# Optimization experiments

Measured on AMD Instinct MI355X. Metric: run time of the kernel, lower is better.

## Reference

```python
import jax, jax.numpy as jnp
import numpy as np

B, S, C, H, W = 8, 32, 3, 256, 256


def setup_inputs() -> dict:
    key = jax.random.key(0)
    k1, k2 = jax.random.split(key)
    return {
        "input": jax.random.normal(k1, (B, S, C, H, W), dtype=jnp.float32),
        "target": jax.random.normal(k2, (B, C, H, W), dtype=jnp.float32),
    }


def _l2norm(x, axis):
    # F.normalize: x / max(||x||_2, eps)
    return x / jnp.maximum(jnp.linalg.norm(x, axis=axis, keepdims=True), 1e-12)


def _forward(input, target):
    b, s, c, h, w = input.shape
    # target: [B,C,H,W] -> permute(0,1,3,2) -> [B,C,W,H] -> flatten(1,2) -> [B, C*W, H]
    target_f = _l2norm(jnp.transpose(target, (0, 1, 3, 2)).reshape(b, c * w, h), axis=1)
    # input: [B,S,C,H,W] -> permute(0,1,2,4,3) -> [B,S,C,W,H] -> flatten(2,3) -> [B,S,C*W,H]
    input_f = _l2norm(jnp.transpose(input, (0, 1, 2, 4, 3)).reshape(b, s, c * w, h), axis=2)

    def corr_one(xf, wf):
        # xf: [S, C*W, H] as conv batch, wf: [C*W, H] as single-output-channel kernel
        y = jax.lax.conv_general_dilated(
            xf, wf[None], window_strides=(1,), padding=[(h - 1, h - 1)],
            dimension_numbers=("NCH", "OIH", "NCH"))
        return y[:, 0, :h]  # first H shift positions (overlap sizes 1..H)

    corr = jax.vmap(corr_one)(input_f, target_f)  # [B, S, H]
    corr = corr / jnp.arange(1, h + 1, dtype=input.dtype)  # mean over overlap size

    overlap = jnp.argmax(corr, axis=-1)            # [B, S] best overlap per sample
    shift = (h - 1) - overlap                      # rows to shift up by

    # out[b,s,:,r,:] = input[b,s,:,r+shift,:] for r < overlap, else 0
    h_idx = jnp.arange(h)[None, None, :] + shift[:, :, None]  # [B, S, H]
    valid = h_idx < h
    idx = jnp.clip(h_idx, 0, h - 1)[:, :, None, :, None]      # [B,S,1,H,1]
    gathered = jnp.take_along_axis(input, idx, axis=3)
    return jnp.where(valid[:, :, None, :, None], gathered, jnp.zeros((), input.dtype))


def reference(input, target):
    return _forward(input, target)
```

## Files before the change

### kernel.cpp

```cpp
#include <hip/hip_runtime.h>

#define B_ 8
#define S_ 32
#define C_ 3
#define H_ 256
#define W_ 256
#define HW_ (H_*W_)
#define CHW_ (C_*H_*W_)
#define NT_ 24
#define TILE_ELEMS 8192

typedef __attribute__((ext_vector_type(8))) short bf16x8;
typedef __attribute__((ext_vector_type(4))) float f32x4;
typedef unsigned int u32;
typedef u32 __attribute__((address_space(3)))* lds_u32p;
typedef const u32 __attribute__((address_space(1)))* glb_u32p;

__device__ __forceinline__ void split2(float x, float y, unsigned &hp, unsigned &lp) {
  unsigned ux = __float_as_uint(x), uy = __float_as_uint(y);
  unsigned hx = ux & 0xFFFF0000u, hy = uy & 0xFFFF0000u;
  float lx = x - __uint_as_float(hx);
  float ly = y - __uint_as_float(hy);
  hp = (ux >> 16) | hy;
  lp = (__float_as_uint(lx) >> 16) | (__float_as_uint(ly) & 0xFFFF0000u);
}

__device__ __forceinline__ void gl2lds16(const ushort* g, ushort* l) {
  __builtin_amdgcn_global_load_lds((glb_u32p)g, (lds_u32p)l, 16, 0, 0);
}

__global__ void ct_ntg(const float* __restrict__ target, float* __restrict__ rntg) {
  int r = (int)((blockIdx.x * (size_t)blockDim.x + threadIdx.x) >> 6);
  int lane = threadIdx.x & 63;
  const float* base = target + (size_t)(r >> 8) * CHW_ + (size_t)(r & 255) * W_;
  float ss = 0.f;
#pragma unroll
  for (int c = 0; c < C_; ++c)
#pragma unroll
    for (int tt = 0; tt < W_/64; ++tt) {
      float v = base[c*HW_ + tt*64 + lane];
      ss = fmaf(v, v, ss);
    }
#pragma unroll
  for (int off = 32; off; off >>= 1) ss += __shfl_xor(ss, off);
  if (lane == 0) rntg[r] = 1.0f / fmaxf(sqrtf(ss), 1e-12f);
}

__global__ void ct_bsplit(const float* __restrict__ target,
                          ushort* __restrict__ BhG, ushort* __restrict__ BlG) {
  int bx = blockIdx.x;
  int b  = bx / 24, kt = bx % 24;
  int c  = kt >> 3, w0 = (kt & 7) * 32;
  int t  = threadIdx.x;
  int trow = t >> 3, tw = t & 7;
  const float* base = target + (size_t)(b*C_ + c) * HW_ + w0 + tw*4;
  ushort* oh = BhG + (size_t)bx * TILE_ELEMS;
  ushort* ol = BlG + (size_t)bx * TILE_ELEMS;
#pragma unroll
  for (int i = 0; i < 8; ++i) {
    int row = trow + 32*i;
    float4 v = *(const float4*)(base + (size_t)row * W_);
    unsigned h0, l0, h1, l1;
    split2(v.x, v.y, h0, l0); split2(v.z, v.w, h1, l1);
    int idx = (row>>4)*512 + (tw>>1)*128 + (row&15)*8 + (tw&1)*4;
    *(uint2*)&oh[idx] = make_uint2(h0, h1);
    *(uint2*)&ol[idx] = make_uint2(l0, l1);
  }
}

__global__ __launch_bounds__(512)
void ct_corr_mfma(const float* __restrict__ input,
                  const ushort* __restrict__ BhG, const ushort* __restrict__ BlG,
                  const float* __restrict__ rntg_g,
                  int* __restrict__ shift_out) {
  __shared__ ushort AhL[2][TILE_ELEMS], AlL[2][TILE_ELEMS];
  __shared__ ushort BhL[2][TILE_ELEMS], BlL[2][TILE_ELEMS];
  __shared__ float ninSq[256], rnin[256], rntg_s[256], corrS[256];
  __shared__ unsigned long long wkey[4];

  const int bs = blockIdx.x;
  const int bG = bs >> 5;
  const int t  = threadIdx.x;
  const int lane = t & 63;
  const int wid  = t >> 6;
  const int wm   = wid >> 2;
  const int wn   = wid & 3;

  const float* Abase = input + (size_t)bs * CHW_;

  if (t < 256) { ninSq[t] = 0.f; corrS[t] = 0.f; rntg_s[t] = rntg_g[bG*256 + t]; }

  f32x4 acc[8][4];
#pragma unroll
  for (int m = 0; m < 8; ++m)
#pragma unroll
    for (int n = 0; n < 4; ++n) acc[m][n] = (f32x4){0.f, 0.f, 0.f, 0.f};

  float4 paE[4], paO[4];
  float ssA[4] = {0.f, 0.f, 0.f, 0.f};

#define ISSUE_A(KT, PA) {                                                     \
    const float* Ab = Abase + (size_t)((KT) >> 3) * HW_ + ((KT) & 7) * 32;    \
    _Pragma("unroll")                                                         \
    for (int p = 0; p < 4; ++p) {                                             \
      int f = p*512 + t;                                                      \
      int row = (f >> 7) * 16 + ((f >> 1) & 15);                              \
      int kk  = ((f >> 5) & 3) * 8 + (f & 1) * 4;                             \
      PA[p] = *(const float4*)(Ab + (size_t)row * W_ + kk);                   \
    } }

#define ISSUE_B(KT, NXP) {                                                    \
    const ushort* gh = BhG + (size_t)(bG*NT_ + (KT)) * TILE_ELEMS + wn*2048;  \
    const ushort* gl = BlG + (size_t)(bG*NT_ + (KT)) * TILE_ELEMS + wn*2048;  \
    _Pragma("unroll")                                                         \
    for (int o = 0; o < 4; ++o)                                               \
      gl2lds16(gh + o*512 + lane*8, &BhL[NXP][wn*2048 + o*512]);              \
    _Pragma("unroll")                                                         \
    for (int o = 0; o < 4; ++o)                                               \
      gl2lds16(gl + o*512 + lane*8, &BlL[NXP][wn*2048 + o*512]);              \
    __builtin_amdgcn_sched_barrier(0); }

#define STASH_A(PA, NXP) {                                                    \
    _Pragma("unroll")                                                         \
    for (int p = 0; p < 4; ++p) {                                             \
      int f = p*512 + t;                                                      \
      int idx = (f>>7)*512 + ((f>>5)&3)*128 + ((f>>1)&15)*8 + (f&1)*4;        \
      float4 va = PA[p];                                                      \
      ssA[p] = fmaf(va.x, va.x, fmaf(va.y, va.y,                              \
               fmaf(va.z, va.z, fmaf(va.w, va.w, ssA[p]))));                  \
      unsigned h0, l0, h1, l1;                                                \
      split2(va.x, va.y, h0, l0); split2(va.z, va.w, h1, l1);                 \
      *(uint2*)&AhL[NXP][idx] = make_uint2(h0, h1);                           \
      *(uint2*)&AlL[NXP][idx] = make_uint2(l0, l1);                           \
    } }

#define MFMA_BODY(CURP) {                                                     \
    bf16x8 bh[4], bl[4];                                                      \
    _Pragma("unroll")                                                         \
    for (int n = 0; n < 4; ++n) {                                             \
      int ct = wn*4 + n;                                                      \
      bh[n] = *(const bf16x8*)&BhL[CURP][ct*512 + lane*8];                    \
      bl[n] = *(const bf16x8*)&BlL[CURP][ct*512 + lane*8];                    \
    }                                                                         \
    __builtin_amdgcn_s_setprio(1);                                            \
    _Pragma("unroll")                                                         \
    for (int m = 0; m < 8; ++m) {                                             \
      int rt = wm*8 + m;                                                      \
      bf16x8 ah = *(const bf16x8*)&AhL[CURP][rt*512 + lane*8];                \
      bf16x8 al = *(const bf16x8*)&AlL[CURP][rt*512 + lane*8];                \
      _Pragma("unroll")                                                       \
      for (int n = 0; n < 4; ++n) {                                           \
        acc[m][n] = __builtin_amdgcn_mfma_f32_16x16x32_bf16(ah, bh[n], acc[m][n], 0, 0, 0); \
        acc[m][n] = __builtin_amdgcn_mfma_f32_16x16x32_bf16(ah, bl[n], acc[m][n], 0, 0, 0); \
        acc[m][n] = __builtin_amdgcn_mfma_f32_16x16x32_bf16(al, bh[n], acc[m][n], 0, 0, 0); \
      }                                                                       \
    }                                                                         \
    __builtin_amdgcn_s_setprio(0); }

#define WAIT_VM4() { asm volatile("s_waitcnt vmcnt(4)" ::: "memory");         \
                     __builtin_amdgcn_sched_barrier(0); }
#define WAIT_VM0() { asm volatile("s_waitcnt vmcnt(0)" ::: "memory");         \
                     __builtin_amdgcn_sched_barrier(0); }
#define BAR() { asm volatile("s_waitcnt lgkmcnt(0)" ::: "memory");            \
                __builtin_amdgcn_sched_barrier(0);                            \
                __builtin_amdgcn_s_barrier();                                 \
                __builtin_amdgcn_sched_barrier(0); }

  ISSUE_A(0, paE);
  __builtin_amdgcn_sched_barrier(0);
  ISSUE_B(0, 0);
  ISSUE_A(1, paO);
  __builtin_amdgcn_sched_barrier(0);
  STASH_A(paE, 0);
  BAR();

#define TILE_EVEN(KT, DO_A) {                                                 \
    WAIT_VM4();                                                               \
    ISSUE_B((KT)+1, 1);                                                       \
    MFMA_BODY(0);                                                             \
    STASH_A(paO, 1);                                                          \
    if (DO_A) { ISSUE_A((KT)+2, paE); }                                       \
    BAR(); }
#define TILE_ODD(KT) {                                                        \
    WAIT_VM4();                                                               \
    ISSUE_B((KT)+1, 0);                                                       \
    MFMA_BODY(1);                                                             \
    STASH_A(paE, 0);                                                          \
    ISSUE_A((KT)+2, paO);                                                     \
    BAR(); }

  for (int it = 0; it < 11; ++it) {
    int k0 = 2*it;
    TILE_EVEN(k0, true);
    TILE_ODD(k0 + 1);
  }
  TILE_EVEN(22, false);
  WAIT_VM0();
  MFMA_BODY(1);

#pragma unroll
  for (int p = 0; p < 4; ++p) {
    int row = (p*4 + (t >> 7)) * 16 + ((t >> 1) & 15);
    atomicAdd(&ninSq[row], ssA[p]);
  }
  __syncthreads();
  if (t < 256) rnin[t] = 1.0f / fmaxf(sqrtf(ninSq[t]), 1e-12f);
  __syncthreads();

#pragma unroll
  for (int n = 0; n < 4; ++n) {
    int col = wn*64 + n*16 + (lane & 15);
    float rc = rntg_s[col];
#pragma unroll
    for (int m = 0; m < 8; ++m) {
      f32x4 a = acc[m][n];
#pragma unroll
      for (int r = 0; r < 4; ++r) {
        int row = wm*128 + m*16 + (lane >> 4)*4 + r;
        int q = col - row;
        if (q >= 0) atomicAdd(&corrS[q], a[r] * rnin[row] * rc);
      }
    }
  }
  __syncthreads();

  if (t < 256) {
    int q = 255 - t;
    float v = corrS[q] / (float)(256 - q);
    unsigned u = __float_as_uint(v);
    u = (u & 0x80000000u) ? ~u : (u | 0x80000000u);
    unsigned long long key = ((unsigned long long)u << 32) | (unsigned)q;
#pragma unroll
    for (int off = 32; off; off >>= 1) {
      unsigned long long o = __shfl_xor(key, off);
      if (o > key) key = o;
    }
    if ((t & 63) == 0) wkey[t >> 6] = key;
  }
  __syncthreads();
  if (t == 0) {
    unsigned long long k = wkey[0];
#pragma unroll
    for (int i = 1; i < 4; ++i) if (wkey[i] > k) k = wkey[i];
    shift_out[bs] = (int)(k & 0xFFFFFFFFull);
  }
}

__global__ void ct_gather(const float* __restrict__ input,
                          const int* __restrict__ shift,
                          float* __restrict__ out) {
  size_t idx = (size_t)blockIdx.x * blockDim.x + threadIdx.x;
  int w4 = (int)(idx & 63);
  int h  = (int)((idx >> 6) & 255);
  int sc = (int)(idx >> 14);
  int bs = sc / 3;
  int hh = h + shift[bs];
  float4 v = make_float4(0.f, 0.f, 0.f, 0.f);
  if (hh < H_) v = *(const float4*)(input + ((size_t)sc << 16) + (size_t)hh * W_ + w4*4);
  *(float4*)(out + (idx << 2)) = v;
}

extern "C" void kernel_launch(void* const* d_in, const int* in_sizes, int n_in,
                              void* d_out, int out_size, void* d_ws, size_t ws_size,
                              hipStream_t stream) {
  const float* input  = (const float*)d_in[0];
  const float* target = (const float*)d_in[1];
  float* out = (float*)d_out;

  float* rntg = (float*)d_ws;
  int* shift  = (int*)(rntg + 2048);
  ushort* BhG = (ushort*)(shift + 256);
  ushort* BlG = BhG + (size_t)B_ * NT_ * TILE_ELEMS;

  ct_ntg       <<<512, 256, 0, stream>>>(target, rntg);
  ct_bsplit    <<<B_ * NT_, 256, 0, stream>>>(target, BhG, BlG);
  ct_corr_mfma <<<B_ * S_, 512, 0, stream>>>(input, BhG, BlG, rntg, shift);
  ct_gather    <<<(B_*S_*C_*H_*W_/4) / 256, 256, 0, stream>>>(input, shift, out);
}
```

Before: 172.5 us.

## Split correlation GEMM across four row-blocks per sample with global atomic reduction

```diff
diff --git a/kernel.cpp b/kernel.cpp
--- a/kernel.cpp
+++ b/kernel.cpp
@@ -27,6 +27,11 @@
 
 __device__ __forceinline__ void gl2lds16(const ushort* g, ushort* l) {
   __builtin_amdgcn_global_load_lds((glb_u32p)g, (lds_u32p)l, 16, 0, 0);
+}
+
+__global__ void ct_zero(float* __restrict__ corrG) {
+  int i = blockIdx.x * 256 + threadIdx.x;
+  *(float4*)(corrG + i * 4) = make_float4(0.f, 0.f, 0.f, 0.f);
 }
 
 __global__ void ct_ntg(const float* __restrict__ target, float* __restrict__ rntg) {
@@ -68,182 +73,169 @@
   }
 }
 
-__global__ __launch_bounds__(512)
+__global__ __launch_bounds__(256, 3)
 void ct_corr_mfma(const float* __restrict__ input,
                   const ushort* __restrict__ BhG, const ushort* __restrict__ BlG,
                   const float* __restrict__ rntg_g,
-                  int* __restrict__ shift_out) {
-  __shared__ ushort AhL[2][TILE_ELEMS], AlL[2][TILE_ELEMS];
-  __shared__ ushort BhL[2][TILE_ELEMS], BlL[2][TILE_ELEMS];
-  __shared__ float ninSq[256], rnin[256], rntg_s[256], corrS[256];
-  __shared__ unsigned long long wkey[4];
-
-  const int bs = blockIdx.x;
+                  float* __restrict__ corrG) {
+  __shared__ ushort AhL[2048], AlL[2048];
+  __shared__ ushort BhL[8192], BlL[8192];
+  __shared__ float ninSq[64], rnin[64], corrS[256];
+
+  const int bx = blockIdx.x;
+  const int bs = bx >> 2;
+  const int mb = bx & 3;
   const int bG = bs >> 5;
   const int t  = threadIdx.x;
   const int lane = t & 63;
   const int wid  = t >> 6;
-  const int wm   = wid >> 2;
-  const int wn   = wid & 3;
-
-  const float* Abase = input + (size_t)bs * CHW_;
-
-  if (t < 256) { ninSq[t] = 0.f; corrS[t] = 0.f; rntg_s[t] = rntg_g[bG*256 + t]; }
-
-  f32x4 acc[8][4];
-#pragma unroll
-  for (int m = 0; m < 8; ++m)
+  const int cp   = mb + wid;
+  const bool act = (cp < 4);
+
+  const float* Abase = input + (size_t)bs * CHW_ + (size_t)(mb * 64) * W_;
+
+  if (t < 64) ninSq[t] = 0.f;
+  corrS[t] = 0.f;
+
+  f32x4 acc[4][4];
+#pragma unroll
+  for (int m = 0; m < 4; ++m)
 #pragma unroll
     for (int n = 0; n < 4; ++n) acc[m][n] = (f32x4){0.f, 0.f, 0.f, 0.f};
 
-  float4 paE[4], paO[4];
-  float ssA[4] = {0.f, 0.f, 0.f, 0.f};
-
-#define ISSUE_A(KT, PA) {                                                     \
+  float4 pa[2];
+  float ssA[2] = {0.f, 0.f};
+
+#define ISSUE_A(KT) {                                                         \
     const float* Ab = Abase + (size_t)((KT) >> 3) * HW_ + ((KT) & 7) * 32;    \
     _Pragma("unroll")                                                         \
-    for (int p = 0; p < 4; ++p) {                                             \
-      int f = p*512 + t;                                                      \
-      int row = (f >> 7) * 16 + ((f >> 1) & 15);                              \
-      int kk  = ((f >> 5) & 3) * 8 + (f & 1) * 4;                             \
-      PA[p] = *(const float4*)(Ab + (size_t)row * W_ + kk);                   \
+    for (int p = 0; p < 2; ++p) {                                             \
+      int f = p*256 + t;                                                      \
+      pa[p] = *(const float4*)(Ab + (size_t)(f >> 3) * W_ + (f & 7) * 4);     \
     } }
 
-#define ISSUE_B(KT, NXP) {                                                    \
-    const ushort* gh = BhG + (size_t)(bG*NT_ + (KT)) * TILE_ELEMS + wn*2048;  \
-    const ushort* gl = BlG + (size_t)(bG*NT_ + (KT)) * TILE_ELEMS + wn*2048;  \
-    _Pragma("unroll")                                                         \
-    for (int o = 0; o < 4; ++o)                                               \
-      gl2lds16(gh + o*512 + lane*8, &BhL[NXP][wn*2048 + o*512]);              \
-    _Pragma("unroll")                                                         \
-    for (int o = 0; o < 4; ++o)                                               \
-      gl2lds16(gl + o*512 + lane*8, &BlL[NXP][wn*2048 + o*512]);              \
-    __builtin_amdgcn_sched_barrier(0); }
-
-#define STASH_A(PA, NXP) {                                                    \
-    _Pragma("unroll")                                                         \
-    for (int p = 0; p < 4; ++p) {                                             \
-      int f = p*512 + t;                                                      \
-      int idx = (f>>7)*512 + ((f>>5)&3)*128 + ((f>>1)&15)*8 + (f&1)*4;        \
-      float4 va = PA[p];                                                      \
+#define STASH_A() {                                                           \
+    _Pragma("unroll")                                                         \
+    for (int p = 0; p < 2; ++p) {                                             \
+      int f = p*256 + t;                                                      \
+      int row = f >> 3, kk = (f & 7) * 4;                                     \
+      int idx = (row>>4)*512 + (kk>>3)*128 + (row&15)*8 + (kk&4);             \
+      float4 va = pa[p];                                                      \
       ssA[p] = fmaf(va.x, va.x, fmaf(va.y, va.y,                              \
                fmaf(va.z, va.z, fmaf(va.w, va.w, ssA[p]))));                  \
       unsigned h0, l0, h1, l1;                                                \
       split2(va.x, va.y, h0, l0); split2(va.z, va.w, h1, l1);                 \
-      *(uint2*)&AhL[NXP][idx] = make_uint2(h0, h1);                           \
-      *(uint2*)&AlL[NXP][idx] = make_uint2(l0, l1);                           \
+      *(uint2*)&AhL[idx] = make_uint2(h0, h1);                                \
+      *(uint2*)&AlL[idx] = make_uint2(l0, l1);                                \
     } }
 
-#define MFMA_BODY(CURP) {                                                     \
-    bf16x8 bh[4], bl[4];                                                      \
-    _Pragma("unroll")                                                         \
-    for (int n = 0; n < 4; ++n) {                                             \
-      int ct = wn*4 + n;                                                      \
-      bh[n] = *(const bf16x8*)&BhL[CURP][ct*512 + lane*8];                    \
-      bl[n] = *(const bf16x8*)&BlL[CURP][ct*512 + lane*8];                    \
-    }                                                                         \
-    __builtin_amdgcn_s_setprio(1);                                            \
-    _Pragma("unroll")                                                         \
-    for (int m = 0; m < 8; ++m) {                                             \
-      int rt = wm*8 + m;                                                      \
-      bf16x8 ah = *(const bf16x8*)&AhL[CURP][rt*512 + lane*8];                \
-      bf16x8 al = *(const bf16x8*)&AlL[CURP][rt*512 + lane*8];                \
-      _Pragma("unroll")                                                       \
-      for (int n = 0; n < 4; ++n) {                                           \
-        acc[m][n] = __builtin_amdgcn_mfma_f32_16x16x32_bf16(ah, bh[n], acc[m][n], 0, 0, 0); \
-        acc[m][n] = __builtin_amdgcn_mfma_f32_16x16x32_bf16(ah, bl[n], acc[m][n], 0, 0, 0); \
-        acc[m][n] = __builtin_amdgcn_mfma_f32_16x16x32_bf16(al, bh[n], acc[m][n], 0, 0, 0); \
-      }                                                                       \
-    }                                                                         \
-    __builtin_amdgcn_s_setprio(0); }
-
-#define WAIT_VM4() { asm volatile("s_waitcnt vmcnt(4)" ::: "memory");         \
-                     __builtin_amdgcn_sched_barrier(0); }
-#define WAIT_VM0() { asm volatile("s_waitcnt vmcnt(0)" ::: "memory");         \
-                     __builtin_amdgcn_sched_barrier(0); }
-#define BAR() { asm volatile("s_waitcnt lgkmcnt(0)" ::: "memory");            \
-                __builtin_amdgcn_sched_barrier(0);                            \
-                __builtin_amdgcn_s_barrier();                                 \
-                __builtin_amdgcn_sched_barrier(0); }
-
-  ISSUE_A(0, paE);
-  __builtin_amdgcn_sched_barrier(0);
-  ISSUE_B(0, 0);
-  ISSUE_A(1, paO);
-  __builtin_amdgcn_sched_barrier(0);
-  STASH_A(paE, 0);
-  BAR();
-
-#define TILE_EVEN(KT, DO_A) {                                                 \
-    WAIT_VM4();                                                               \
-    ISSUE_B((KT)+1, 1);                                                       \
-    MFMA_BODY(0);                                                             \
-    STASH_A(paO, 1);                                                          \
-    if (DO_A) { ISSUE_A((KT)+2, paE); }                                       \
-    BAR(); }
-#define TILE_ODD(KT) {                                                        \
-    WAIT_VM4();                                                               \
-    ISSUE_B((KT)+1, 0);                                                       \
-    MFMA_BODY(1);                                                             \
-    STASH_A(paE, 0);                                                          \
-    ISSUE_A((KT)+2, paO);                                                     \
-    BAR(); }
-
-  for (int it = 0; it < 11; ++it) {
-    int k0 = 2*it;
-    TILE_EVEN(k0, true);
-    TILE_ODD(k0 + 1);
-  }
-  TILE_EVEN(22, false);
-  WAIT_VM0();
-  MFMA_BODY(1);
-
-#pragma unroll
-  for (int p = 0; p < 4; ++p) {
-    int row = (p*4 + (t >> 7)) * 16 + ((t >> 1) & 15);
+#define ISSUE_B(KT) if (act) {                                                \
+    const ushort* gh = BhG + (size_t)(bG*NT_ + (KT)) * TILE_ELEMS + cp*2048;  \
+    const ushort* gl = BlG + (size_t)(bG*NT_ + (KT)) * TILE_ELEMS + cp*2048;  \
+    _Pragma("unroll")                                                         \
+    for (int o = 0; o < 4; ++o)                                               \
+      gl2lds16(gh + o*512 + lane*8, &BhL[cp*2048 + o*512]);                   \
+    _Pragma("unroll")                                                         \
+    for (int o = 0; o < 4; ++o)                                               \
+      gl2lds16(gl + o*512 + lane*8, &BlL[cp*2048 + o*512]);                   \
+  }
+
+#define SBAR0() __builtin_amdgcn_sched_barrier(0)
+
+  ISSUE_A(0);
+  SBAR0();
+
+  for (int kt = 0; kt < NT_; ++kt) {
+    SBAR0();
+    __builtin_amdgcn_s_barrier();
+    SBAR0();
+    ISSUE_B(kt);
+    SBAR0();
+    STASH_A();
+    SBAR0();
+    if (kt < NT_ - 1) { ISSUE_A(kt + 1); }
+    SBAR0();
+    asm volatile("s_waitcnt lgkmcnt(0)" ::: "memory");
+    if (kt < NT_ - 1) { asm volatile("s_waitcnt vmcnt(2)" ::: "memory"); }
+    else              { asm volatile("s_waitcnt vmcnt(0)" ::: "memory"); }
+    SBAR0();
+    __builtin_amdgcn_s_barrier();
+    SBAR0();
+
+    if (act) {
+      bf16x8 bh[4], bl[4];
+#pragma unroll
+      for (int n = 0; n < 4; ++n) {
+        int ct = cp*4 + n;
+        bh[n] = *(const bf16x8*)&BhL[ct*512 + lane*8];
+        bl[n] = *(const bf16x8*)&BlL[ct*512 + lane*8];
+      }
+      __builtin_amdgcn_s_setprio(1);
+#pragma unroll
+      for (int m = 0; m < 4; ++m) {
+        bf16x8 ah = *(const bf16x8*)&AhL[m*512 + lane*8];
+        bf16x8 al = *(const bf16x8*)&AlL[m*512 + lane*8];
+#pragma unroll
+        for (int n = 0; n < 4; ++n) {
+          acc[m][n] = __builtin_amdgcn_mfma_f32_16x16x32_bf16(ah, bh[n], acc[m][n], 0, 0, 0);
+          acc[m][n] = __builtin_amdgcn_mfma_f32_16x16x32_bf16(ah, bl[n], acc[m][n], 0, 0, 0);
+          acc[m][n] = __builtin_amdgcn_mfma_f32_16x16x32_bf16(al, bh[n], acc[m][n], 0, 0, 0);
+        }
+      }
+      __builtin_amdgcn_s_setprio(0);
+    }
+  }
+
+#pragma unroll
+  for (int p = 0; p < 2; ++p) {
+    int row = (p*256 + t) >> 3;
     atomicAdd(&ninSq[row], ssA[p]);
   }
   __syncthreads();
-  if (t < 256) rnin[t] = 1.0f / fmaxf(sqrtf(ninSq[t]), 1e-12f);
+  if (t < 64) rnin[t] = 1.0f / fmaxf(sqrtf(ninSq[t]), 1e-12f);
   __syncthreads();
 
-#pragma unroll
-  for (int n = 0; n < 4; ++n) {
-    int col = wn*64 + n*16 + (lane & 15);
-    float rc = rntg_s[col];
-#pragma unroll
-    for (int m = 0; m < 8; ++m) {
-      f32x4 a = acc[m][n];
-#pragma unroll
-      for (int r = 0; r < 4; ++r) {
-        int row = wm*128 + m*16 + (lane >> 4)*4 + r;
-        int q = col - row;
-        if (q >= 0) atomicAdd(&corrS[q], a[r] * rnin[row] * rc);
+  if (act) {
+#pragma unroll
+    for (int n = 0; n < 4; ++n) {
+      int col = cp*64 + n*16 + (lane & 15);
+      float rc = rntg_g[bG*256 + col];
+#pragma unroll
+      for (int m = 0; m < 4; ++m) {
+        f32x4 a = acc[m][n];
+#pragma unroll
+        for (int r = 0; r < 4; ++r) {
+          int lrow = m*16 + (lane >> 4)*4 + r;
+          int q = col - (mb*64 + lrow);
+          if (q >= 0) atomicAdd(&corrS[q], a[r] * rnin[lrow] * rc);
+        }
       }
     }
   }
   __syncthreads();
 
-  if (t < 256) {
-    int q = 255 - t;
-    float v = corrS[q] / (float)(256 - q);
+  atomicAdd(&corrG[bs*256 + t], corrS[t]);
+}
+
+__global__ void ct_argmax(const float* __restrict__ corrG, int* __restrict__ shift) {
+  int bs = blockIdx.x;
+  int lane = threadIdx.x;
+  unsigned long long key = 0;
+#pragma unroll
+  for (int i = 0; i < 4; ++i) {
+    int q = lane + 64*i;
+    float v = corrG[bs*256 + q] / (float)(256 - q);
     unsigned u = __float_as_uint(v);
     u = (u & 0x80000000u) ? ~u : (u | 0x80000000u);
-    unsigned long long key = ((unsigned long long)u << 32) | (unsigned)q;
-#pragma unroll
-    for (int off = 32; off; off >>= 1) {
-      unsigned long long o = __shfl_xor(key, off);
-      if (o > key) key = o;
-    }
-    if ((t & 63) == 0) wkey[t >> 6] = key;
-  }
-  __syncthreads();
-  if (t == 0) {
-    unsigned long long k = wkey[0];
-#pragma unroll
-    for (int i = 1; i < 4; ++i) if (wkey[i] > k) k = wkey[i];
-    shift_out[bs] = (int)(k & 0xFFFFFFFFull);
-  }
+    unsigned long long k = ((unsigned long long)u << 32) | (unsigned)q;
+    if (k > key) key = k;
+  }
+#pragma unroll
+  for (int off = 32; off; off >>= 1) {
+    unsigned long long o = __shfl_xor(key, off);
+    if (o > key) key = o;
+  }
+  if (lane == 0) shift[bs] = (int)(key & 0xFFFFFFFFull);
 }
 
 __global__ void ct_gather(const float* __restrict__ input,
@@ -267,13 +259,16 @@
   const float* target = (const float*)d_in[1];
   float* out = (float*)d_out;
 
-  float* rntg = (float*)d_ws;
-  int* shift  = (int*)(rntg + 2048);
-  ushort* BhG = (ushort*)(shift + 256);
-  ushort* BlG = BhG + (size_t)B_ * NT_ * TILE_ELEMS;
-
+  float* rntg  = (float*)d_ws;
+  float* corrG = rntg + 2048;
+  int*   shift = (int*)(corrG + 65536);
+  ushort* BhG  = (ushort*)(shift + 256);
+  ushort* BlG  = BhG + (size_t)B_ * NT_ * TILE_ELEMS;
+
+  ct_zero      <<<64, 256, 0, stream>>>(corrG);
   ct_ntg       <<<512, 256, 0, stream>>>(target, rntg);
   ct_bsplit    <<<B_ * NT_, 256, 0, stream>>>(target, BhG, BlG);
-  ct_corr_mfma <<<B_ * S_, 512, 0, stream>>>(input, BhG, BlG, rntg, shift);
+  ct_corr_mfma <<<B_ * S_ * 4, 256, 0, stream>>>(input, BhG, BlG, rntg, corrG);
+  ct_argmax    <<<B_ * S_, 64, 0, stream>>>(corrG, shift);
   ct_gather    <<<(B_*S_*C_*H_*W_/4) / 256, 256, 0, stream>>>(input, shift, out);
 }
```

New measurement: 238.8 us. +38.4%, slower.
